# Kernel optimization log

Hardware: AMD Instinct MI355X
Metric: run time of the kernel (lower is better)

## Reference

```python
import jax, jax.numpy as jnp
import numpy as np
from jax import lax

B, S, D, H = 512, 120, 216, 1024
MAX_LEN = 24


def setup_inputs() -> dict:
    key = jax.random.key(0)
    ks = jax.random.split(key, 8)
    u = lambda k, shape: jax.random.uniform(k, shape, jnp.float32, -0.08, 0.08)  # init_weights
    return {
        "src": jax.random.normal(ks[0], (B, S, D), jnp.float32),
        "W_ih": u(ks[1], (4 * H, D)),
        "W_hh": u(ks[2], (4 * H, H)),
        "b_ih": u(ks[3], (4 * H,)),
        "b_hh": u(ks[4], (4 * H,)),
        "W_out": u(ks[5], (D, H)),
        "b_out": u(ks[6], (D,)),
        "max_len": MAX_LEN,
    }


def _lstm_cell(x, h, c, W_ih, W_hh, b):
    # PyTorch gate order: i, f, g, o
    gates = x @ W_ih.T + h @ W_hh.T + b  # (B, 4H)
    i, f, g, o = jnp.split(gates, 4, axis=-1)
    c_new = jax.nn.sigmoid(f) * c + jax.nn.sigmoid(i) * jnp.tanh(g)
    h_new = jax.nn.sigmoid(o) * jnp.tanh(c_new)
    return h_new, c_new


def reference(src, W_ih, W_hh, b_ih, b_hh, W_out, b_out, max_len):
    # Eval-mode forward: dropout off; encoder teacher-forced over src;
    b = b_ih + b_hh
    src_t = jnp.swapaxes(src, 0, 1)  # (S, B, D)
    Bsz = src.shape[0]
    Hd = W_hh.shape[1]
    h0 = jnp.zeros((Bsz, Hd), src.dtype)
    c0 = jnp.zeros((Bsz, Hd), src.dtype)

    def enc_step(carry, x_t):
        h, c = carry
        h, c = _lstm_cell(x_t, h, c, W_ih, W_hh, b)
        return (h, c), None

    (h, c), _ = lax.scan(enc_step, (h0, c0), src_t)

    def dec_step(carry, _):
        h, c, inp = carry
        h, c = _lstm_cell(inp, h, c, W_ih, W_hh, b)
        y = h @ W_out.T + b_out  # project_to_output
        return (h, c, y), y

    (_, _, _), ys = lax.scan(dec_step, (h, c, src_t[-1]), None, length=max_len)
    return jnp.swapaxes(ys, 0, 1)  # (B, max_len, D)
```

## Files before the change

### kernel.cpp

```cpp
#include <hip/hip_runtime.h>
#include <cstdint>
#include <cstddef>

#define B_SZ 512
#define S_SZ 120
#define D_SZ 216
#define H_SZ 1024
#define NG   4096
#define DP   256
#define KENC 1280
#define TMAX 24

#define BM 64
#define BN 128
#define BK 64
#define NBUF 5

using bf16_t = __bf16;
using bf16x8 = __attribute__((ext_vector_type(8))) __bf16;
using f32x4  = __attribute__((ext_vector_type(4))) float;

__device__ __forceinline__ void gload16(const void* g, void* l) {
  __builtin_amdgcn_global_load_lds(
      (const __attribute__((address_space(1))) void*)g,
      (__attribute__((address_space(3))) void*)l, 16, 0, 0);
}
__device__ __forceinline__ void gload16c(const void* g, void* l) {
  __builtin_amdgcn_global_load_lds(
      (const __attribute__((address_space(1))) void*)g,
      (__attribute__((address_space(3))) void*)l, 16, 0, 0x11);
}

__device__ __forceinline__ float fsigmoid(float x) {
  x = fminf(fmaxf(x, -30.f), 30.f);
  return 1.f / (1.f + __expf(-x));
}
__device__ __forceinline__ float ftanh(float x) {
  x = fminf(fmaxf(x, -15.f), 15.f);
  float e = __expf(2.f * x);
  return (e - 1.f) / (e + 1.f);
}

#define BUFB 24576

struct __align__(16) SmemChain {
  bf16_t stage[NBUF][(BM + BN) * BK];
  float gate[BM * 132];
};

struct __align__(16) SmemG {
  union {
    bf16_t stage[3][(BM + BN) * BK];
    float gate[BM * 129];
  };
};

__global__ __launch_bounds__(512, 1) void lstm_chain(
    const bf16_t* __restrict__ srcbf,
    const bf16_t* __restrict__ Wcat,
    const bf16_t* __restrict__ Wdec,
    const float* __restrict__ biasE,
    const float* __restrict__ biasD,
    bf16_t* __restrict__ hA,
    bf16_t* __restrict__ hB,
    bf16_t* __restrict__ Hs,
    unsigned* __restrict__ flags)
{
  __shared__ SmemChain sm;
  const int t    = threadIdx.x;
  const int bid  = blockIdx.x;
  const int n0   = (bid & 31) * BN;
  const int m0   = (bid >> 5) * BM;
  const int lane = t & 63;
  const int wv   = t >> 6;
  const int wm   = wv >> 2;
  const int wn   = wv & 3;
  const int fr   = lane & 15;
  const int fq   = lane >> 4;

  char* ldsbase = (char*)&sm.stage[0][0];

  const int sgrp = lane >> 3;
  const int sw8  = (((lane & 7) ^ sgrp) & 7) * 8;
  const int aRowOff = 8 * wv + sgrp;
  const int wRowOff = 16 * wv + sgrp;

  const int swz   = fr & 7;
  const int co0   = ((fq) ^ swz) * 16;
  const int co1   = ((4 + fq) ^ swz) * 16;
  const int arow0 = (wm * 32 + fr) * 128;
  const int arow1 = (wm * 32 + 16 + fr) * 128;
  const int brow  = 8192 + (wn * 32 + fr) * 128;
  const int u0    = n0 >> 2;

  const int panel = m0 >> 6;
  unsigned* flg = flags + panel * 32;
  unsigned* myf = flg + (n0 >> 7);
  const unsigned* myFlagAddr = flg + (lane & 31);

  auto stageSlice = [&](const bf16_t* Ab, int sA, int ka, bool coh,
                        const bf16_t* Wb, int sW2, int kw, int buf) {
    char* lb = ldsbase + buf * BUFB;
    const bf16_t* ap = Ab + (size_t)(m0 + aRowOff) * sA + sw8 + ka;
    if (coh) gload16c(ap, lb + wv * 1024);
    else     gload16 (ap, lb + wv * 1024);
    const bf16_t* wp = Wb + (size_t)(n0 + wRowOff) * sW2 + sw8 + kw;
    gload16(wp, lb + 8192 + wv * 2048);
    gload16(wp + (size_t)8 * sW2, lb + 8192 + wv * 2048 + 1024);
  };

  f32x4 acc[2][2];

  auto compute = [&](int bf) {
    const char* Lb = ldsbase + bf * BUFB;
#pragma unroll
    for (int kk = 0; kk < 2; ++kk) {
      const int co = kk ? co1 : co0;
      bf16x8 av0 = *(const bf16x8*)(Lb + arow0 + co);
      bf16x8 av1 = *(const bf16x8*)(Lb + arow1 + co);
      bf16x8 bv0 = *(const bf16x8*)(Lb + brow + co);
      bf16x8 bv1 = *(const bf16x8*)(Lb + brow + 2048 + co);
      acc[0][0] = __builtin_amdgcn_mfma_f32_16x16x32_bf16(av0, bv0, acc[0][0], 0, 0, 0);
      acc[0][1] = __builtin_amdgcn_mfma_f32_16x16x32_bf16(av0, bv1, acc[0][1], 0, 0, 0);
      acc[1][0] = __builtin_amdgcn_mfma_f32_16x16x32_bf16(av1, bv0, acc[1][0], 0, 0, 0);
      acc[1][1] = __builtin_amdgcn_mfma_f32_16x16x32_bf16(av1, bv1, acc[1][1], 0, 0, 0);
    }
  };

  auto panelSpin = [&](unsigned need) {
    for (;;) {
      unsigned v;
      asm volatile("global_load_dword %0, %1, off sc0 sc1\n\t"
                   "s_waitcnt vmcnt(0)"
                   : "=v"(v) : "v"(myFlagAddr) : "memory");
      if (__all((int)(v >= need))) break;
      __builtin_amdgcn_s_sleep(2);
    }
  };

  float c4[4] = {0.f, 0.f, 0.f, 0.f};
  float biasE2[2], biasD2[2];
#pragma unroll
  for (int j = 0; j < 2; ++j) {
    int col = n0 + wn * 32 + j * 16 + fr;
    biasE2[j] = biasE[col];
    biasD2[j] = biasD[col];
  }

  const bf16_t* hprev = hA;
  int cb = 0;

  stageSlice(srcbf, DP, 0,      false, Wcat, KENC, 0,      0);
  stageSlice(srcbf, DP, BK,     false, Wcat, KENC, BK,     1);
  stageSlice(srcbf, DP, 2 * BK, false, Wcat, KENC, 2 * BK, 2);
  stageSlice(srcbf, DP, 3 * BK, false, Wcat, KENC, 3 * BK, 3);

#pragma clang loop unroll(disable)
  for (int s = 0; s < 144; ++s) {
    const bool enc = (s <= 120);
    const int  xi  = (s < 120) ? s : 119;
    const bf16_t* Asrc = srcbf + (size_t)xi * B_SZ * DP;
    const int n1 = enc ? (DP / BK) : 0;
    const bf16_t* Wb  = enc ? Wcat : Wdec;
    const int     sWb = enc ? KENC : H_SZ;
    bf16_t* hnext = (s < 120) ? ((s & 1) ? hA : hB)
                              : (Hs + (size_t)(s - 120) * B_SZ * H_SZ);
    const int nTot = n1 + H_SZ / BK;

    float bias2[2];
#pragma unroll
    for (int j = 0; j < 2; ++j) bias2[j] = enc ? biasE2[j] : biasD2[j];

#pragma unroll
    for (int i = 0; i < 2; ++i)
#pragma unroll
      for (int j = 0; j < 2; ++j) acc[i][j] = (f32x4){0.f, 0.f, 0.f, 0.f};

    for (int it = 0; it < nTot; ++it) {
      const int rem = nTot - it;
      if (rem >= 4)
        asm volatile("s_waitcnt vmcnt(9)" ::: "memory");
      else if (rem == 3)
        asm volatile("s_waitcnt vmcnt(6)" ::: "memory");
      else if (rem == 2)
        asm volatile("s_waitcnt vmcnt(3)" ::: "memory");
      else
        asm volatile("s_waitcnt vmcnt(0)" ::: "memory");
      __builtin_amdgcn_s_barrier();

      const int j4 = it + 4;
      if (j4 < nTot) {
        int sbuf = cb + 4; if (sbuf >= NBUF) sbuf -= NBUF;
        if (j4 < n1) stageSlice(Asrc, DP, j4 * BK, false, Wb, sWb, j4 * BK, sbuf);
        else         stageSlice(hprev, H_SZ, (j4 - n1) * BK, true, Wb, sWb, j4 * BK, sbuf);
      }

      compute(cb);
      cb = (cb == NBUF - 1) ? 0 : cb + 1;
    }

#pragma unroll
    for (int i = 0; i < 2; ++i)
#pragma unroll
      for (int j = 0; j < 2; ++j)
#pragma unroll
        for (int v = 0; v < 4; ++v) {
          int row = wm * 32 + i * 16 + fq * 4 + v;
          int col = wn * 32 + j * 16 + fr;
          sm.gate[row * 132 + col] = acc[i][j][v] + bias2[j];
        }
    __syncthreads();
#pragma unroll
    for (int itc = 0; itc < 4; ++itc) {
      int ci  = itc * 512 + t;
      int brw = ci >> 5;
      int ju  = ci & 31;
      f32x4 g = *(const f32x4*)&sm.gate[brw * 132 + ju * 4];
      float iv = fsigmoid(g[0]);
      float fv = fsigmoid(g[1]);
      float gv = ftanh(g[2]);
      float ov = fsigmoid(g[3]);
      float cn = fv * c4[itc] + iv * gv;
      c4[itc] = cn;
      bf16_t hb = (bf16_t)(ov * ftanh(cn));
      uint32_t hv32 = (uint32_t)__builtin_bit_cast(uint16_t, hb);
      size_t cix = (size_t)(m0 + brw) * H_SZ + (u0 + ju);
      asm volatile("global_store_short %0, %1, off sc0 sc1"
                   :: "v"((uint16_t*)&hnext[cix]), "v"(hv32) : "memory");
    }
    asm volatile("s_waitcnt vmcnt(0)" ::: "memory");
    __syncthreads();
    if (t == 0) {
      unsigned fv2 = (unsigned)(s + 1);
      asm volatile("global_store_dword %0, %1, off sc0 sc1"
                   :: "v"(myf), "v"(fv2) : "memory");
    }

    if (s < 143) {
      const bool nxtEnc = (s + 1 <= 120);
      if (nxtEnc) {
        const bf16_t* nxtA = srcbf + (size_t)((s + 1 < 120) ? (s + 1) : 119) * B_SZ * DP;
        int b = cb;
#pragma unroll
        for (int q = 0; q < 4; ++q) {
          stageSlice(nxtA, DP, q * BK, false, Wcat, KENC, q * BK, b);
          b = (b == NBUF - 1) ? 0 : b + 1;
        }
        panelSpin((unsigned)(s + 1));
      } else {
        panelSpin((unsigned)(s + 1));
        int b = cb;
#pragma unroll
        for (int q = 0; q < 4; ++q) {
          stageSlice(hnext, H_SZ, q * BK, true, Wdec, H_SZ, q * BK, b);
          b = (b == NBUF - 1) ? 0 : b + 1;
        }
      }
    }

    hprev = hnext;
  }
}

template <int EPI>
__global__ __launch_bounds__(256, 1) void gemm_step(
    const bf16_t* __restrict__ A1, int sA1, int n1,
    const bf16_t* __restrict__ A2, int sA2, int n2,
    const bf16_t* __restrict__ W, int sW,
    const float* __restrict__ bias,
    float* __restrict__ cbuf, bf16_t* __restrict__ hout,
    const float* __restrict__ addm, bf16_t* __restrict__ outb,
    float* __restrict__ outf)
{
  __shared__ SmemG sm;
  const int t    = threadIdx.x;
  const int m0   = blockIdx.y * BM;
  const int n0   = blockIdx.x * BN;
  const int lane = t & 63;
  const int wv   = t >> 6;
  const int wm   = wv >> 1, wn = wv & 1;
  const int fr   = lane & 15;
  const int fq   = lane >> 4;

  f32x4 acc[2][4] = {};

  float bias4[4];
  if (EPI == 1 || EPI == 3) {
#pragma unroll
    for (int j = 0; j < 4; ++j) {
      int col = n0 + wn * 64 + j * 16 + fr;
      bias4[j] = (EPI == 3 && col >= D_SZ) ? 0.f : bias[col];
    }
  }

  const int r0   = t >> 3;
  const int gcol = (((t & 7) ^ (r0 & 7)) * 8);
  char* ldsbase  = (char*)&sm.stage[0][0];
  const int wofs = wv * 1024;

  const bf16_t* pA1 = A1 ? A1 : A2;
  const bf16_t* pA2 = A2 ? A2 : A1;
  const bf16_t* a1p0 = pA1 + (size_t)(m0 + r0) * sA1 + gcol;
  const bf16_t* a1p1 = pA1 + (size_t)(m0 + r0 + 32) * sA1 + gcol;
  const bf16_t* a2p0 = pA2 + (size_t)(m0 + r0) * sA2 + gcol;
  const bf16_t* a2p1 = pA2 + (size_t)(m0 + r0 + 32) * sA2 + gcol;
  const bf16_t* wp0  = W + (size_t)(n0 + r0) * sW + gcol;
  const bf16_t* wp1  = W + (size_t)(n0 + r0 + 32) * sW + gcol;
  const bf16_t* wp2  = W + (size_t)(n0 + r0 + 64) * sW + gcol;
  const bf16_t* wp3  = W + (size_t)(n0 + r0 + 96) * sW + gcol;

  const int nTot = n1 + n2;

  auto stage = [&](int j, int bf) {
    char* Ab = ldsbase + bf * BUFB + wofs;
    char* Bb = ldsbase + bf * BUFB + 8192 + wofs;
    const int k = j * BK;
    const bf16_t *a0, *a1;
    if (j < n1) { a0 = a1p0 + k; a1 = a1p1 + k; }
    else { const int k2 = k - n1 * BK; a0 = a2p0 + k2; a1 = a2p1 + k2; }
    gload16(a0, Ab);
    gload16(a1, Ab + 4096);
    gload16(wp0 + k, Bb);
    gload16(wp1 + k, Bb + 4096);
    gload16(wp2 + k, Bb + 8192);
    gload16(wp3 + k, Bb + 12288);
  };

  const int swz  = fr & 7;
  const int co0  = ((fq) ^ swz) * 16;
  const int co1  = ((4 + fq) ^ swz) * 16;
  const int arow0 = (wm * 32 + fr) * 128;
  const int arow1 = (wm * 32 + 16 + fr) * 128;
  const int brow  = (wn * 64 + fr) * 128;

  auto compute = [&](int bf) {
    const char* Ab = ldsbase + bf * BUFB;
    const char* Bb = Ab + 8192;
#pragma unroll
    for (int kk = 0; kk < 2; ++kk) {
      const int co = kk ? co1 : co0;
      bf16x8 av0 = *(const bf16x8*)(Ab + arow0 + co);
      bf16x8 av1 = *(const bf16x8*)(Ab + arow1 + co);
      bf16x8 bv[4];
#pragma unroll
      for (int j = 0; j < 4; ++j)
        bv[j] = *(const bf16x8*)(Bb + brow + j * 2048 + co);
#pragma unroll
      for (int j = 0; j < 4; ++j) {
        acc[0][j] = __builtin_amdgcn_mfma_f32_16x16x32_bf16(av0, bv[j], acc[0][j], 0, 0, 0);
        acc[1][j] = __builtin_amdgcn_mfma_f32_16x16x32_bf16(av1, bv[j], acc[1][j], 0, 0, 0);
      }
    }
  };

  stage(0, 0);
  if (nTot > 1) stage(1, 1);
  int cb = 0, sb = 2;
  for (int it = 0; it < nTot; ++it) {
    if (it == nTot - 1) {
      asm volatile("s_waitcnt vmcnt(0)" ::: "memory");
    } else {
      asm volatile("s_waitcnt vmcnt(6)" ::: "memory");
    }
    __builtin_amdgcn_s_barrier();
    if (it + 2 < nTot) stage(it + 2, sb);
    sb = (sb == 2) ? 0 : sb + 1;
    compute(cb);
    cb = (cb == 2) ? 0 : cb + 1;
  }
  __syncthreads();

  if (EPI == 1) {
#pragma unroll
    for (int i = 0; i < 2; ++i)
#pragma unroll
      for (int j = 0; j < 4; ++j)
#pragma unroll
        for (int v = 0; v < 4; ++v) {
          int row = wm * 32 + i * 16 + fq * 4 + v;
          int col = wn * 64 + j * 16 + fr;
          sm.gate[row * 129 + col] = acc[i][j][v] + bias4[j];
        }
    __syncthreads();
    const int u0 = n0 >> 2;
#pragma unroll
    for (int itc = 0; itc < 8; ++itc) {
      int ci = itc * 256 + t;
      int brw = ci >> 5;
      int ju  = ci & 31;
      const float* gp = &sm.gate[brw * 129 + ju * 4];
      float iv = fsigmoid(gp[0]);
      float fv = fsigmoid(gp[1]);
      float gv = ftanh(gp[2]);
      float ov = fsigmoid(gp[3]);
      size_t cix = (size_t)(m0 + brw) * H_SZ + (u0 + ju);
      float cn = fv * cbuf[cix] + iv * gv;
      cbuf[cix] = cn;
      hout[cix] = (bf16_t)(ov * ftanh(cn));
    }
  }

  if (EPI == 2) {
#pragma unroll
    for (int i = 0; i < 2; ++i)
#pragma unroll
      for (int j = 0; j < 4; ++j)
#pragma unroll
        for (int v = 0; v < 4; ++v) {
          int gr = m0 + wm * 32 + i * 16 + fq * 4 + v;
          int gc = n0 + wn * 64 + j * 16 + fr;
          int orig = (gr & 3) * H_SZ + (gr >> 2);
          float val = acc[i][j][v] + addm[(size_t)orig * H_SZ + gc];
          outb[(size_t)gr * H_SZ + gc] = (bf16_t)val;
        }
  }

  if (EPI == 3) {
#pragma unroll
    for (int i = 0; i < 2; ++i)
#pragma unroll
      for (int j = 0; j < 4; ++j)
#pragma unroll
        for (int v = 0; v < 4; ++v) {
          int m = m0 + wm * 32 + i * 16 + fq * 4 + v;
          int n = n0 + wn * 64 + j * 16 + fr;
          if (n < D_SZ) {
            int ts = m >> 9;
            int bb = m & 511;
            outf[((size_t)bb * TMAX + ts) * D_SZ + n] = acc[i][j][v] + bias4[j];
          }
        }
  }
}

__global__ void k_convert_src(const float* __restrict__ src, bf16_t* __restrict__ dst) {
  int idx = blockIdx.x * 256 + threadIdx.x;
  int total = S_SZ * B_SZ * DP;
  if (idx >= total) return;
  int d = idx % DP;
  int r = idx / DP;
  int b = r % B_SZ;
  int tt = r / B_SZ;
  float v = (d < D_SZ) ? src[((size_t)b * S_SZ + tt) * D_SZ + d] : 0.f;
  dst[idx] = (bf16_t)v;
}

__global__ void k_build_wcat(const float* __restrict__ Wih, const float* __restrict__ Whh,
                             bf16_t* __restrict__ Wcat) {
  int idx = blockIdx.x * 256 + threadIdx.x;
  if (idx >= NG * KENC) return;
  int k = idx % KENC;
  int r = idx / KENC;
  int o = (r & 3) * H_SZ + (r >> 2);
  float v;
  if (k < D_SZ)      v = Wih[(size_t)o * D_SZ + k];
  else if (k < DP)   v = 0.f;
  else               v = Whh[(size_t)o * H_SZ + (k - DP)];
  Wcat[idx] = (bf16_t)v;
}

__global__ void k_build_wout(const float* __restrict__ Wout, bf16_t* __restrict__ WoutB,
                             bf16_t* __restrict__ WoutT) {
  int idx = blockIdx.x * 256 + threadIdx.x;
  if (idx < 256 * H_SZ) {
    int h = idx % H_SZ, d = idx / H_SZ;
    WoutB[idx] = (bf16_t)((d < D_SZ) ? Wout[(size_t)d * H_SZ + h] : 0.f);
  }
  if (idx < H_SZ * DP) {
    int d = idx % DP, h = idx / DP;
    WoutT[idx] = (bf16_t)((d < D_SZ) ? Wout[(size_t)d * H_SZ + h] : 0.f);
  }
}

__global__ void k_build_bias(const float* __restrict__ bih, const float* __restrict__ bhh,
                             const float* __restrict__ Wih, const float* __restrict__ bout,
                             float* __restrict__ biasE, float* __restrict__ biasD) {
  int r = blockIdx.x * 256 + threadIdx.x;
  if (r >= NG) return;
  int o = (r & 3) * H_SZ + (r >> 2);
  float be = bih[o] + bhh[o];
  biasE[r] = be;
  float s = 0.f;
  const float* wr = Wih + (size_t)o * D_SZ;
  for (int d = 0; d < D_SZ; ++d) s += wr[d] * bout[d];
  biasD[r] = be + s;
}

extern "C" void kernel_launch(void* const* d_in, const int* in_sizes, int n_in,
                              void* d_out, int out_size, void* d_ws, size_t ws_size,
                              hipStream_t stream) {
  const float* src  = (const float*)d_in[0];
  const float* Wih  = (const float*)d_in[1];
  const float* Whh  = (const float*)d_in[2];
  const float* bih  = (const float*)d_in[3];
  const float* bhh  = (const float*)d_in[4];
  const float* Wout = (const float*)d_in[5];
  const float* bout = (const float*)d_in[6];

  char* ws = (char*)d_ws;
  size_t off = 0;
  auto alloc = [&](size_t bytes) {
    void* p = ws + off;
    off = (off + bytes + 255) & ~(size_t)255;
    return p;
  };
  bf16_t* srcbf = (bf16_t*)alloc((size_t)S_SZ * B_SZ * DP * 2);
  bf16_t* Wcat  = (bf16_t*)alloc((size_t)NG * KENC * 2);
  bf16_t* Wdec  = (bf16_t*)alloc((size_t)NG * H_SZ * 2);
  bf16_t* WoutB = (bf16_t*)alloc((size_t)256 * H_SZ * 2);
  bf16_t* WoutT = (bf16_t*)alloc((size_t)H_SZ * DP * 2);
  float*  biasE = (float*)alloc((size_t)NG * 4);
  float*  biasD = (float*)alloc((size_t)NG * 4);
  float*  cbuf  = (float*)alloc((size_t)B_SZ * H_SZ * 4);
  bf16_t* hP0   = (bf16_t*)alloc((size_t)B_SZ * H_SZ * 2);
  bf16_t* hP1   = (bf16_t*)alloc((size_t)B_SZ * H_SZ * 2);
  bf16_t* Hs    = (bf16_t*)alloc((size_t)TMAX * B_SZ * H_SZ * 2);
  unsigned* flags = (unsigned*)alloc(1024);

  hipMemsetAsync(hP0, 0, (size_t)B_SZ * H_SZ * 2, stream);
  hipMemsetAsync(flags, 0, 1024, stream);

  k_convert_src<<<(S_SZ * B_SZ * DP + 255) / 256, 256, 0, stream>>>(src, srcbf);
  k_build_wcat<<<(NG * KENC + 255) / 256, 256, 0, stream>>>(Wih, Whh, Wcat);
  k_build_wout<<<1024, 256, 0, stream>>>(Wout, WoutB, WoutT);
  k_build_bias<<<(NG + 255) / 256, 256, 0, stream>>>(bih, bhh, Wih, bout, biasE, biasD);

  gemm_step<2><<<dim3(H_SZ / BN, NG / BM), 256, 0, stream>>>(
      Wcat, KENC, DP / BK, nullptr, 0, 0, WoutT, DP,
      nullptr, nullptr, nullptr, Whh, Wdec, nullptr);

  {
    const bf16_t* a_src = srcbf;
    const bf16_t* a_wc  = Wcat;
    const bf16_t* a_wd  = Wdec;
    const float*  a_bE  = biasE;
    const float*  a_bD  = biasD;
    bf16_t*       a_hA  = hP0;
    bf16_t*       a_hB  = hP1;
    bf16_t*       a_Hs  = Hs;
    unsigned*     a_fl  = flags;
    void* kargs[] = {&a_src, &a_wc, &a_wd, &a_bE, &a_bD,
                     &a_hA, &a_hB, &a_Hs, &a_fl};
    hipLaunchCooperativeKernel((void*)lstm_chain, dim3(256), dim3(512),
                               kargs, 0, stream);
  }

  gemm_step<3><<<dim3(2, (TMAX * B_SZ) / BM), 256, 0, stream>>>(
      nullptr, 0, 0, Hs, H_SZ, H_SZ / BK, WoutB, H_SZ,
      bout, nullptr, nullptr, nullptr, nullptr, (float*)d_out);
}
```

Before: 1.731 ms.

## Split K across wave pairs with larger per-wave tiles in LSTM chain kernel

Reorganizes the persistent LSTM kernel so each wave computes a 32x64 output tile with 8 MFMAs per k-slice, and wave pairs split the K dimension by handling alternate k-slices, then reduce their partial sums through LDS. Staging goes from 5 to 6 buffers and advances two slices per barrier, and the gate scratch buffer reuses a staging buffer instead of a separate LDS region. The aim is to halve barriers per step and raise MFMA density per LDS fragment load. The cost is an extra LDS reduction pass and more synchronisation in the epilogue. The loop also now stages only from hprev after the prologue, which assumes the src slices all fit in the 4 prefetched slices.

```diff
diff --git a/kernel.cpp b/kernel.cpp
--- a/kernel.cpp
+++ b/kernel.cpp
@@ -14,7 +14,7 @@
 #define BM 64
 #define BN 128
 #define BK 64
-#define NBUF 5
+#define NBUF 6
 
 using bf16_t = __bf16;
 using bf16x8 = __attribute__((ext_vector_type(8))) __bf16;
@@ -45,7 +45,6 @@
 
 struct __align__(16) SmemChain {
   bf16_t stage[NBUF][(BM + BN) * BK];
-  float gate[BM * 132];
 };
 
 struct __align__(16) SmemG {
@@ -73,8 +72,10 @@
   const int m0   = (bid >> 5) * BM;
   const int lane = t & 63;
   const int wv   = t >> 6;
-  const int wm   = wv >> 2;
-  const int wn   = wv & 3;
+  const int kg   = wv & 1;
+  const int wt   = wv >> 1;
+  const int tm   = wt >> 1;
+  const int tn   = wt & 1;
   const int fr   = lane & 15;
   const int fq   = lane >> 4;
 
@@ -88,9 +89,9 @@
   const int swz   = fr & 7;
   const int co0   = ((fq) ^ swz) * 16;
   const int co1   = ((4 + fq) ^ swz) * 16;
-  const int arow0 = (wm * 32 + fr) * 128;
-  const int arow1 = (wm * 32 + 16 + fr) * 128;
-  const int brow  = 8192 + (wn * 32 + fr) * 128;
+  const int arow0 = (tm * 32 + fr) * 128;
+  const int arow1 = (tm * 32 + 16 + fr) * 128;
+  const int brow  = 8192 + (tn * 64 + fr) * 128;
   const int u0    = n0 >> 2;
 
   const int panel = m0 >> 6;
@@ -109,7 +110,7 @@
     gload16(wp + (size_t)8 * sW2, lb + 8192 + wv * 2048 + 1024);
   };
 
-  f32x4 acc[2][2];
+  f32x4 acc[2][4];
 
   auto compute = [&](int bf) {
     const char* Lb = ldsbase + bf * BUFB;
@@ -118,12 +119,15 @@
       const int co = kk ? co1 : co0;
       bf16x8 av0 = *(const bf16x8*)(Lb + arow0 + co);
       bf16x8 av1 = *(const bf16x8*)(Lb + arow1 + co);
-      bf16x8 bv0 = *(const bf16x8*)(Lb + brow + co);
-      bf16x8 bv1 = *(const bf16x8*)(Lb + brow + 2048 + co);
-      acc[0][0] = __builtin_amdgcn_mfma_f32_16x16x32_bf16(av0, bv0, acc[0][0], 0, 0, 0);
-      acc[0][1] = __builtin_amdgcn_mfma_f32_16x16x32_bf16(av0, bv1, acc[0][1], 0, 0, 0);
-      acc[1][0] = __builtin_amdgcn_mfma_f32_16x16x32_bf16(av1, bv0, acc[1][0], 0, 0, 0);
-      acc[1][1] = __builtin_amdgcn_mfma_f32_16x16x32_bf16(av1, bv1, acc[1][1], 0, 0, 0);
+      bf16x8 bv[4];
+#pragma unroll
+      for (int j = 0; j < 4; ++j)
+        bv[j] = *(const bf16x8*)(Lb + brow + j * 2048 + co);
+#pragma unroll
+      for (int j = 0; j < 4; ++j) {
+        acc[0][j] = __builtin_amdgcn_mfma_f32_16x16x32_bf16(av0, bv[j], acc[0][j], 0, 0, 0);
+        acc[1][j] = __builtin_amdgcn_mfma_f32_16x16x32_bf16(av1, bv[j], acc[1][j], 0, 0, 0);
+      }
     }
   };
 
@@ -139,16 +143,16 @@
   };
 
   float c4[4] = {0.f, 0.f, 0.f, 0.f};
-  float biasE2[2], biasD2[2];
-#pragma unroll
-  for (int j = 0; j < 2; ++j) {
-    int col = n0 + wn * 32 + j * 16 + fr;
-    biasE2[j] = biasE[col];
-    biasD2[j] = biasD[col];
+  float biasE4[4], biasD4[4];
+#pragma unroll
+  for (int j = 0; j < 4; ++j) {
+    int col = n0 + tn * 64 + j * 16 + fr;
+    biasE4[j] = biasE[col];
+    biasD4[j] = biasD[col];
   }
 
   const bf16_t* hprev = hA;
-  int cb = 0;
+  int b0 = 0;
 
   stageSlice(srcbf, DP, 0,      false, Wcat, KENC, 0,      0);
   stageSlice(srcbf, DP, BK,     false, Wcat, KENC, BK,     1);
@@ -158,64 +162,85 @@
 #pragma clang loop unroll(disable)
   for (int s = 0; s < 144; ++s) {
     const bool enc = (s <= 120);
-    const int  xi  = (s < 120) ? s : 119;
-    const bf16_t* Asrc = srcbf + (size_t)xi * B_SZ * DP;
     const int n1 = enc ? (DP / BK) : 0;
     const bf16_t* Wb  = enc ? Wcat : Wdec;
     const int     sWb = enc ? KENC : H_SZ;
     bf16_t* hnext = (s < 120) ? ((s & 1) ? hA : hB)
                               : (Hs + (size_t)(s - 120) * B_SZ * H_SZ);
-    const int nTot = n1 + H_SZ / BK;
-
-    float bias2[2];
-#pragma unroll
-    for (int j = 0; j < 2; ++j) bias2[j] = enc ? biasE2[j] : biasD2[j];
+    const int nTot   = n1 + H_SZ / BK;
+    const int npairs = nTot >> 1;
+
+    float bias4[4];
+#pragma unroll
+    for (int j = 0; j < 4; ++j) bias4[j] = enc ? biasE4[j] : biasD4[j];
 
 #pragma unroll
     for (int i = 0; i < 2; ++i)
 #pragma unroll
-      for (int j = 0; j < 2; ++j) acc[i][j] = (f32x4){0.f, 0.f, 0.f, 0.f};
-
-    for (int it = 0; it < nTot; ++it) {
-      const int rem = nTot - it;
-      if (rem >= 4)
-        asm volatile("s_waitcnt vmcnt(9)" ::: "memory");
-      else if (rem == 3)
-        asm volatile("s_waitcnt vmcnt(6)" ::: "memory");
-      else if (rem == 2)
-        asm volatile("s_waitcnt vmcnt(3)" ::: "memory");
-      else
-        asm volatile("s_waitcnt vmcnt(0)" ::: "memory");
+      for (int j = 0; j < 4; ++j) acc[i][j] = (f32x4){0.f, 0.f, 0.f, 0.f};
+
+    int cbm = b0 + kg;          if (cbm >= NBUF) cbm -= NBUF;
+    int sb  = b0 + 4;           if (sb  >= NBUF) sb  -= NBUF;
+
+    for (int p = 0; p < npairs; ++p) {
+      if (p < npairs - 1) {
+        if (kg == 0) asm volatile("s_waitcnt vmcnt(9)" ::: "memory");
+        else         asm volatile("s_waitcnt vmcnt(6)" ::: "memory");
+      } else {
+        if (kg == 0) asm volatile("s_waitcnt vmcnt(3)" ::: "memory");
+        else         asm volatile("s_waitcnt vmcnt(0)" ::: "memory");
+      }
       __builtin_amdgcn_s_barrier();
 
-      const int j4 = it + 4;
-      if (j4 < nTot) {
-        int sbuf = cb + 4; if (sbuf >= NBUF) sbuf -= NBUF;
-        if (j4 < n1) stageSlice(Asrc, DP, j4 * BK, false, Wb, sWb, j4 * BK, sbuf);
-        else         stageSlice(hprev, H_SZ, (j4 - n1) * BK, true, Wb, sWb, j4 * BK, sbuf);
+      const int js = 2 * p + 4;
+      if (js < nTot) {
+        stageSlice(hprev, H_SZ, (js - n1) * BK, true, Wb, sWb, js * BK, sb);
+        int sb2 = sb + 1; if (sb2 >= NBUF) sb2 -= NBUF;
+        stageSlice(hprev, H_SZ, (js + 1 - n1) * BK, true, Wb, sWb, (js + 1) * BK, sb2);
+        sb = sb2 + 1; if (sb >= NBUF) sb -= NBUF;
       }
 
-      compute(cb);
-      cb = (cb == NBUF - 1) ? 0 : cb + 1;
-    }
-
-#pragma unroll
-    for (int i = 0; i < 2; ++i)
-#pragma unroll
-      for (int j = 0; j < 2; ++j)
-#pragma unroll
-        for (int v = 0; v < 4; ++v) {
-          int row = wm * 32 + i * 16 + fq * 4 + v;
-          int col = wn * 32 + j * 16 + fr;
-          sm.gate[row * 132 + col] = acc[i][j][v] + bias2[j];
-        }
+      compute(cbm);
+      cbm += 2; if (cbm >= NBUF) cbm -= NBUF;
+    }
+
+    const int gbuf = (b0 + nTot + 4) % NBUF;
+    float* gate = (float*)(ldsbase + gbuf * BUFB);
     __syncthreads();
+
+    if (kg == 0) {
+#pragma unroll
+      for (int i = 0; i < 2; ++i)
+#pragma unroll
+        for (int j = 0; j < 4; ++j)
+#pragma unroll
+          for (int v = 0; v < 4; ++v) {
+            int row = tm * 32 + i * 16 + fq * 4 + v;
+            int col = tn * 64 + j * 16 + fr;
+            gate[row * 132 + col] = acc[i][j][v] + bias4[j];
+          }
+    }
+    __syncthreads();
+    if (kg == 1) {
+#pragma unroll
+      for (int i = 0; i < 2; ++i)
+#pragma unroll
+        for (int j = 0; j < 4; ++j)
+#pragma unroll
+          for (int v = 0; v < 4; ++v) {
+            int row = tm * 32 + i * 16 + fq * 4 + v;
+            int col = tn * 64 + j * 16 + fr;
+            gate[row * 132 + col] += acc[i][j][v];
+          }
+    }
+    __syncthreads();
+
 #pragma unroll
     for (int itc = 0; itc < 4; ++itc) {
       int ci  = itc * 512 + t;
       int brw = ci >> 5;
       int ju  = ci & 31;
-      f32x4 g = *(const f32x4*)&sm.gate[brw * 132 + ju * 4];
+      f32x4 g = *(const f32x4*)&gate[brw * 132 + ju * 4];
       float iv = fsigmoid(g[0]);
       float fv = fsigmoid(g[1]);
       float gv = ftanh(g[2]);
@@ -236,11 +261,13 @@
                    :: "v"(myf), "v"(fv2) : "memory");
     }
 
+    int nb0 = b0 + (nTot - ((nTot / NBUF) * NBUF));
+    if (nb0 >= NBUF) nb0 -= NBUF;
     if (s < 143) {
       const bool nxtEnc = (s + 1 <= 120);
       if (nxtEnc) {
         const bf16_t* nxtA = srcbf + (size_t)((s + 1 < 120) ? (s + 1) : 119) * B_SZ * DP;
-        int b = cb;
+        int b = nb0;
 #pragma unroll
         for (int q = 0; q < 4; ++q) {
           stageSlice(nxtA, DP, q * BK, false, Wcat, KENC, q * BK, b);
@@ -249,7 +276,7 @@
         panelSpin((unsigned)(s + 1));
       } else {
         panelSpin((unsigned)(s + 1));
-        int b = cb;
+        int b = nb0;
 #pragma unroll
         for (int q = 0; q < 4; ++q) {
           stageSlice(hnext, H_SZ, q * BK, true, Wdec, H_SZ, q * BK, b);
@@ -258,6 +285,7 @@
       }
     }
 
+    b0 = nb0;
     hprev = hnext;
   }
 }
```

New measurement: 1.720 ms. No clear change (-0.7%).
